# Optimization experiments

Hardware: AMD Instinct MI355X
Metric: run time of the kernel (lower is better)

Reference implementation:

```python
import jax, jax.numpy as jnp
import numpy as np

D = 64        # GatedGraphConv out_channels
N_LAYERS = 5  # number of stacked convs


def setup_inputs() -> dict:
    key = jax.random.key(0)
    ks = jax.random.split(key, 16)
    N, E, G = 100000, 1600000, 64
    s = 0.1
    inp = {
        'conv_weight': jax.random.normal(ks[0], (N_LAYERS, D, D), jnp.float32) * s,
        'gru_w_ih':    jax.random.normal(ks[1], (N_LAYERS, 3 * D, D), jnp.float32) * s,
        'gru_w_hh':    jax.random.normal(ks[2], (N_LAYERS, 3 * D, D), jnp.float32) * s,
        'gru_b_ih':    jax.random.normal(ks[3], (N_LAYERS, 3 * D), jnp.float32) * s,
        'gru_b_hh':    jax.random.normal(ks[4], (N_LAYERS, 3 * D), jnp.float32) * s,
        'fc1_w': jax.random.normal(ks[5], (32, D), jnp.float32) * s,
        'fc1_b': jax.random.normal(ks[6], (32,), jnp.float32) * s,
        'fc2_w': jax.random.normal(ks[7], (16, 32), jnp.float32) * s,
        'fc2_b': jax.random.normal(ks[8], (16,), jnp.float32) * s,
        'fc3_w': jax.random.normal(ks[9], (1, 16), jnp.float32) * s,
        'fc3_b': jax.random.normal(ks[10], (1,), jnp.float32) * s,
        'edge_index': jax.random.randint(ks[11], (2, E), 0, N, jnp.int64 if jax.config.jax_enable_x64 else jnp.int32),
        'batch': jnp.sort(jax.random.randint(ks[12], (N,), 0, G, jnp.int32)),
        'num_nodes': N,
        'num_graphs': G,
    }
    return inp


def _gru_cell(m, h, w_ih, w_hh, b_ih, b_hh):
    # torch.nn.GRUCell math; m: [N,D] input, h: [N,D] hidden
    gi = m @ w_ih.T + b_ih   # [N, 3D]
    gh = h @ w_hh.T + b_hh   # [N, 3D]
    i_r, i_z, i_n = jnp.split(gi, 3, axis=1)
    h_r, h_z, h_n = jnp.split(gh, 3, axis=1)
    r = jax.nn.sigmoid(i_r + h_r)
    z = jax.nn.sigmoid(i_z + h_z)
    n = jnp.tanh(i_n + r * h_n)
    return (1.0 - z) * n + z * h


def reference(conv_weight, gru_w_ih, gru_w_hh, gru_b_ih, gru_b_hh,
              fc1_w, fc1_b, fc2_w, fc2_b, fc3_w, fc3_b,
              edge_index, batch, num_nodes, num_graphs):
    src, dst = edge_index[0], edge_index[1]  # source_to_target flow
    # initial node features: zeros [N,8] zero-padded to D by GatedGraphConv
    x0 = jnp.zeros((num_nodes, D), jnp.float32)

    def step(x, params):
        w, wih, whh, bih, bhh = params
        m = x @ w                                        # [N, D]
        agg = jax.ops.segment_sum(m[src], dst, num_segments=num_nodes)  # scatter-add
        return _gru_cell(agg, x, wih, whh, bih, bhh), None

    x, _ = jax.lax.scan(step, x0,
                        (conv_weight, gru_w_ih, gru_w_hh, gru_b_ih, gru_b_hh))

    # scatter_add pooling over batch -> [num_graphs, D]
    g = jax.ops.segment_sum(x, batch, num_segments=num_graphs)
    h = jax.nn.elu(g @ fc1_w.T + fc1_b)
    h = jax.nn.elu(h @ fc2_w.T + fc2_b)
    return h @ fc3_w.T + fc3_b  # [num_graphs, 1]
```

## Files before the change

kernel.cpp:

```cpp
#include <hip/hip_runtime.h>
#include <math.h>

typedef _Float16 f16x2 __attribute__((ext_vector_type(2)));
typedef _Float16 f16x4 __attribute__((ext_vector_type(4)));
typedef _Float16 f16x8 __attribute__((ext_vector_type(8)));
typedef float f32x4 __attribute__((ext_vector_type(4)));

#define CBITS 10
#define FCHUNK 4096
#define MATSZ 13056
#define SEGSZ 2176
#define TABN 512
__device__ __forceinline__ int woff(int row) { return 64 * row + 8 * (row >> 1); }

__device__ __forceinline__ float sigmoidf_(float v) {
  return 1.0f / (1.0f + __expf(-v));
}
__device__ __forceinline__ float tanhf_(float v) {
  v = fminf(fmaxf(v, -15.f), 15.f);
  float e = __expf(2.f * v);
  return (e - 1.f) / (e + 1.f);
}
__device__ __forceinline__ float eluf_(float v) { return v > 0.f ? v : (__expf(v) - 1.f); }

__global__ __launch_bounds__(256) void histwprep_kernel(const int* __restrict__ dst,
                                                        int* __restrict__ bh, int E, int nfb,
                                                        const float* __restrict__ conv_w,
                                                        const float* __restrict__ w_ih,
                                                        const float* __restrict__ whh,
                                                        const float* __restrict__ b_ih,
                                                        const float* __restrict__ b_hh,
                                                        _Float16* __restrict__ wcS,
                                                        _Float16* __restrict__ whhS,
                                                        _Float16* __restrict__ tab,
                                                        float* __restrict__ gbuf, int gn) {
  __shared__ float sWt[64 * 68];
  __shared__ float sI[48 * 64];
  __shared__ float sh1[64], st[64], su[192], scons[256];
  __shared__ int h[128];
  const int t = threadIdx.x;
  if (blockIdx.x < nfb) {
    if (t < 128) h[t] = 0;
    __syncthreads();
    const int e0 = blockIdx.x * FCHUNK;
    int cnt = E - e0;
    if (cnt > FCHUNK) cnt = FCHUNK;
    for (int i = t; i < cnt; i += 256) atomicAdd(&h[dst[e0 + i] >> CBITS], 1);
    __syncthreads();
    if (t < 128) bh[blockIdx.x * 128 + t] = h[t];
    return;
  }
  const int bid = blockIdx.x - nfb;
  if (bid < 12) {
    const int l = 2 + (bid >> 2);
    const int j0 = (bid & 3) * 48;
    const float* W = conv_w + (size_t)l * 4096;
    const float* wi = w_ih + (size_t)l * 12288;
    _Float16* out = wcS + (size_t)l * MATSZ;
    for (int i = t; i < 4096; i += 256) sWt[(i & 63) * 68 + (i >> 6)] = W[i];
    for (int i = t; i < 3072; i += 256) sI[i] = wi[j0 * 64 + i];
    __syncthreads();
#pragma unroll
    for (int r = 0; r < 3; ++r) {
      int u = t + 256 * r;
      int j = u >> 4, cg = (u & 15) * 4;
      float4 a = {0.f, 0.f, 0.f, 0.f};
      for (int k = 0; k < 64; ++k) {
        float4 w = *(const float4*)(sWt + k * 68 + cg);
        float s = sI[j * 64 + k];
        a.x += w.x * s; a.y += w.y * s; a.z += w.z * s; a.w += w.w * s;
      }
      int row = j0 + j;
      f16x4 hv;
      hv[0] = (_Float16)a.x; hv[1] = (_Float16)a.y;
      hv[2] = (_Float16)a.z; hv[3] = (_Float16)a.w;
      *(f16x4*)(out + woff(row) + cg) = hv;
    }
  } else if (bid < 48) {
    int idx = (bid - 12) * 256 + t;
    if (idx >= 9216) return;
    int l = 2 + idx / 3072, rem = idx % 3072;
    int r = rem >> 4, c4 = (rem & 15) * 4;
    float4 v = *(const float4*)(whh + (size_t)l * 12288 + r * 64 + c4);
    f16x4 hv;
    hv[0] = (_Float16)v.x; hv[1] = (_Float16)v.y;
    hv[2] = (_Float16)v.z; hv[3] = (_Float16)v.w;
    *(f16x4*)(whhS + (size_t)l * MATSZ + woff(r) + c4) = hv;
  } else {
    for (int i = t; i < gn; i += 256) gbuf[i] = 0.f;
    if (t < 64) {
      float r = sigmoidf_(b_ih[t] + b_hh[t]);
      float z = sigmoidf_(b_ih[64 + t] + b_hh[64 + t]);
      float n = tanhf_(b_ih[128 + t] + r * b_hh[128 + t]);
      sh1[t] = (1.f - z) * n;
    }
    __syncthreads();
    if (t < 64) {
      const float* W1 = conv_w + 4096;
      float a = 0.f;
      for (int c = 0; c < 64; ++c) a += sh1[c] * W1[c * 64 + t];
      st[t] = a;
    }
    __syncthreads();
    if (t < 192) {
      const float* wih1 = w_ih + 12288;
      const float* whh1 = whh + 12288;
      float uacc = 0.f, sg = 0.f;
      for (int k = 0; k < 64; ++k) {
        uacc += wih1[t * 64 + k] * st[k];
        sg += whh1[t * 64 + k] * sh1[k];
      }
      su[t] = uacc;
      const float* bi1 = b_ih + 192;
      const float* bh1 = b_hh + 192;
      if (t < 128) {
        scons[t] = sg + bi1[t] + bh1[t];
      } else {
        scons[t] = bi1[t];
        scons[t + 64] = sg + bh1[t];
      }
    }
    __syncthreads();
    for (int idx = t; idx < TABN * 64; idx += 256) {
      int dgi = idx >> 6, j = idx & 63;
      float dg = (float)dgi;
      float r = sigmoidf_(dg * su[j] + scons[j]);
      float z = sigmoidf_(dg * su[64 + j] + scons[64 + j]);
      float n = tanhf_(dg * su[128 + j] + scons[128 + j] + r * scons[192 + j]);
      tab[idx] = (_Float16)(n + z * (sh1[j] - n));
    }
  }
}

__global__ __launch_bounds__(64) void chunkscan_kernel(const int* __restrict__ bh,
                                                       int* __restrict__ cbase,
                                                       int* __restrict__ tot, int nfb) {
  const int b = blockIdx.x;
  const int lane = threadIdx.x;
  int carry = 0;
  for (int base = 0; base < nfb; base += 64) {
    int kk = base + lane;
    int v = (kk < nfb) ? bh[kk * 128 + b] : 0;
    int s = v;
#pragma unroll
    for (int o = 1; o < 64; o <<= 1) {
      int u = __shfl_up(s, o);
      if (lane >= o) s += u;
    }
    if (kk < nfb) cbase[kk * 128 + b] = carry + s - v;
    carry += __shfl(s, 63);
  }
  if (lane == 0) tot[b] = carry;
}

__global__ __launch_bounds__(256) void bucket_fill_kernel(const int* __restrict__ src,
                                                          const int* __restrict__ dst,
                                                          const int* __restrict__ bh,
                                                          const int* __restrict__ cbase,
                                                          const int* __restrict__ tot,
                                                          unsigned* __restrict__ pairs,
                                                          int E) {
  __shared__ uint2 staged[FCHUNK];
  __shared__ int h[128], lbase[128], gbase[128], lcur[128], cs[128];
  const int t = threadIdx.x;
  const int k = blockIdx.x;
  int vtot = 0;
  if (t < 128) {
    vtot = tot[t];
    cs[t] = vtot;
  }
  __syncthreads();
  for (int o = 1; o < 128; o <<= 1) {
    int a = (t < 128 && t >= o) ? cs[t - o] : 0;
    __syncthreads();
    if (t < 128) cs[t] += a;
    __syncthreads();
  }
  if (t < 128) {
    int bucketbase = cs[t] - vtot;
    gbase[t] = bucketbase + cbase[k * 128 + t];
    int myh = bh[k * 128 + t];
    h[t] = myh;
    lcur[t] = myh;
  }
  __syncthreads();
  for (int o = 1; o < 128; o <<= 1) {
    int a = (t < 128 && t >= o) ? lcur[t - o] : 0;
    __syncthreads();
    if (t < 128) lcur[t] += a;
    __syncthreads();
  }
  if (t < 128) {
    int ex = lcur[t] - h[t];
    lbase[t] = ex;
    lcur[t] = ex;
  }
  __syncthreads();
  const int e0 = k * FCHUNK;
  int cnt = E - e0;
  if (cnt > FCHUNK) cnt = FCHUNK;
  for (int i = t; i < cnt; i += 256) {
    int d = dst[e0 + i];
    int b = d >> CBITS;
    int p = atomicAdd(&lcur[b], 1);
    staged[p] = make_uint2((unsigned)src[e0 + i], (unsigned)d);
  }
  __syncthreads();
  for (int i = t; i < cnt; i += 256) {
    uint2 pr = staged[i];
    int b = (int)(pr.y >> CBITS);
    pairs[gbase[b] + (i - lbase[b])] = (pr.x << CBITS) | (pr.y & ((1u << CBITS) - 1));
  }
}

__global__ __launch_bounds__(256) void csr_build_kernel(const unsigned* __restrict__ pairs,
                                                        const int* __restrict__ tot,
                                                        int* __restrict__ offs,
                                                        int* __restrict__ srcs,
                                                        unsigned short* __restrict__ deg16,
                                                        int N, int E) {
  const int b = blockIdx.x, t = threadIdx.x;
  const int nbase = b << CBITS;
  __shared__ int deg[1024];
  __shared__ int ssc[256];
  __shared__ int cs[128];
  if (t < 128) cs[t] = tot[t];
  __syncthreads();
  for (int o = 1; o < 128; o <<= 1) {
    int a = (t < 128 && t >= o) ? cs[t - o] : 0;
    __syncthreads();
    if (t < 128) cs[t] += a;
    __syncthreads();
  }
  const int beg = (b > 0) ? cs[b - 1] : 0;
  const int end = cs[b];
  __syncthreads();
  for (int i = t; i < 1024; i += 256) deg[i] = 0;
  __syncthreads();
  for (int e = beg + t; e < end; e += 256) atomicAdd(&deg[pairs[e] & 1023], 1);
  __syncthreads();
  int d0 = deg[4 * t], d1 = deg[4 * t + 1], d2 = deg[4 * t + 2], d3 = deg[4 * t + 3];
  int s = d0 + d1 + d2 + d3;
  ssc[t] = s;
  __syncthreads();
  for (int o = 1; o < 256; o <<= 1) {
    int a = (t >= o) ? ssc[t - o] : 0;
    __syncthreads();
    ssc[t] += a;
    __syncthreads();
  }
  int base = beg + ssc[t] - s;
  int c0 = base, c1 = c0 + d0, c2 = c1 + d1, c3 = c2 + d2;
  if (nbase + 4 * t + 0 < N) { offs[nbase + 4 * t + 0] = c0; deg16[nbase + 4 * t + 0] = (unsigned short)d0; }
  if (nbase + 4 * t + 1 < N) { offs[nbase + 4 * t + 1] = c1; deg16[nbase + 4 * t + 1] = (unsigned short)d1; }
  if (nbase + 4 * t + 2 < N) { offs[nbase + 4 * t + 2] = c2; deg16[nbase + 4 * t + 2] = (unsigned short)d2; }
  if (nbase + 4 * t + 3 < N) { offs[nbase + 4 * t + 3] = c3; deg16[nbase + 4 * t + 3] = (unsigned short)d3; }
  deg[4 * t] = c0; deg[4 * t + 1] = c1; deg[4 * t + 2] = c2; deg[4 * t + 3] = c3;
  if (b == 0 && t == 0) offs[N] = E;
  if (b == 0 && t < 64) srcs[E + t] = 0;
  __syncthreads();
  for (int e = beg + t; e < end; e += 256) {
    unsigned p = pairs[e];
    int pos = atomicAdd(&deg[p & 1023], 1);
    srcs[pos] = (int)(p >> CBITS);
  }
}

__global__ __launch_bounds__(256) void agg2_kernel(const _Float16* __restrict__ tab,
                                                   const unsigned short* __restrict__ deg16,
                                                   const int* __restrict__ offs,
                                                   const int* __restrict__ srcs,
                                                   _Float16* __restrict__ aggh, int N) {
  int wave = threadIdx.x >> 6, lane = threadIdx.x & 63;
  int v = blockIdx.x * 4 + wave;
  if (v >= N) return;
  const int beg = offs[v], end = offs[v + 1];
  const int deg = end - beg;
  const int og = lane >> 3;
  const int lp = lane & 7;
  f16x8 acc = {};
  for (int base = 0; base < deg; base += 64) {
    const int cnt = min(64, deg - base);
    const int cnt8 = (cnt + 7) & ~7;
    int sidx = 0;
    if (lane < cnt8) sidx = srcs[beg + base + lane];
    int s0 = __shfl(sidx, og);
    int d0 = min((int)deg16[s0], TABN - 1);
    f16x8 cur = *(const f16x8*)(tab + d0 * 64 + lp * 8);
    int e = 0;
    for (; e + 8 < cnt; e += 8) {
      int sn = __shfl(sidx, e + 8 + og);
      int dn = min((int)deg16[sn], TABN - 1);
      f16x8 nxt = *(const f16x8*)(tab + dn * 64 + lp * 8);
      acc += cur;
      cur = nxt;
    }
    if (e + og < cnt) acc += cur;
  }
#pragma unroll
  for (int off = 8; off < 64; off <<= 1) {
    union { f16x8 h; int i[4]; } a, b;
    a.h = acc;
#pragma unroll
    for (int w = 0; w < 4; ++w) b.i[w] = __shfl_xor(a.i[w], off);
    acc += b.h;
  }
  if (og == 0) *(f16x8*)(aggh + (size_t)v * 64 + lp * 8) = acc;
}

__global__ __launch_bounds__(256) void agg_kernel(const _Float16* __restrict__ xh,
                                                  const int* __restrict__ offs,
                                                  const int* __restrict__ srcs,
                                                  _Float16* __restrict__ aggh, int N) {
  int wave = threadIdx.x >> 6, lane = threadIdx.x & 63;
  int v = blockIdx.x * 4 + wave;
  if (v >= N) return;
  const int beg = offs[v], end = offs[v + 1];
  const int deg = end - beg;
  const int og = lane >> 3;
  const int lp = lane & 7;
  f16x8 acc = {};
  for (int base = 0; base < deg; base += 64) {
    const int cnt = min(64, deg - base);
    const int cnt8 = (cnt + 7) & ~7;
    int sidx = 0;
    if (lane < cnt8) sidx = srcs[beg + base + lane];
    int s0 = __shfl(sidx, og);
    f16x8 cur = *(const f16x8*)(xh + (size_t)s0 * 64 + lp * 8);
    int e = 0;
    for (; e + 8 < cnt; e += 8) {
      int sn = __shfl(sidx, e + 8 + og);
      f16x8 nxt = *(const f16x8*)(xh + (size_t)sn * 64 + lp * 8);
      acc += cur;
      cur = nxt;
    }
    if (e + og < cnt) acc += cur;
  }
#pragma unroll
  for (int off = 8; off < 64; off <<= 1) {
    union { f16x8 h; int i[4]; } a, b;
    a.h = acc;
#pragma unroll
    for (int w = 0; w < 4; ++w) b.i[w] = __shfl_xor(a.i[w], off);
    acc += b.h;
  }
  if (og == 0) *(f16x8*)(aggh + (size_t)v * 64 + lp * 8) = acc;
}

template <bool TABH>
__device__ __forceinline__ void gru_body(const _Float16* __restrict__ aggh,
                                         const _Float16* __restrict__ xh_in,
                                         const unsigned short* __restrict__ deg16,
                                         const _Float16* __restrict__ tab,
                                         _Float16* __restrict__ xh_out,
                                         const _Float16* __restrict__ wcS,
                                         const _Float16* __restrict__ whhS,
                                         const float* __restrict__ b_ih,
                                         const float* __restrict__ b_hh,
                                         int N, int tiles) {
  __shared__ _Float16 sW[2 * 3 * SEGSZ];
  const int t = threadIdx.x;
  const int half = blockIdx.x & 1;
  for (int i = t; i < 1632; i += 256) {
    int mat = (i >= 816) ? 1 : 0;
    int rem = i - mat * 816;
    int seg = rem / 272;
    int u = rem % 272;
    const _Float16* srcp = (mat ? whhS : wcS) + woff(half * 32 + seg * 64) + u * 8;
    *(f16x8*)(sW + (mat * 3 + seg) * SEGSZ + u * 8) = *(const f16x8*)srcp;
  }
  __syncthreads();
  const int wave = t >> 6, lane = t & 63;
  const int q = lane >> 4, c = lane & 15;
  float bRZ[2], bZZ[2], bIN[2], bHN[2];
#pragma unroll
  for (int p = 0; p < 2; ++p) {
    int d = (half * 2 + p) * 16 + c;
    bRZ[p] = b_ih[d] + b_hh[d];
    bZZ[p] = b_ih[64 + d] + b_hh[64 + d];
    bIN[p] = b_ih[128 + d];
    bHN[p] = b_hh[128 + d];
  }
  f16x8 idf[2];
#pragma unroll
  for (int p = 0; p < 2; ++p) {
    int tgt = p * 16 + c - q * 8;
#pragma unroll
    for (int j = 0; j < 8; ++j) idf[p][j] = (j == tgt) ? (_Float16)1.0f : (_Float16)0.0f;
  }
#pragma unroll 1
  for (int tile = blockIdx.x >> 1; tile < tiles; tile += gridDim.x >> 1) {
    const int nb0 = tile * 64 + wave * 16;
    const size_t rowbase = (size_t)(nb0 + c) * 64;
    f16x8 aA[2], aH[2];
    if (TABH) {
      int dg = min((int)deg16[nb0 + c], TABN - 1);
#pragma unroll
      for (int ks = 0; ks < 2; ++ks) {
        aA[ks] = *(const f16x8*)(aggh + rowbase + ks * 32 + q * 8);
        aH[ks] = *(const f16x8*)(tab + dg * 64 + ks * 32 + q * 8);
      }
    } else {
#pragma unroll
      for (int ks = 0; ks < 2; ++ks) {
        aA[ks] = *(const f16x8*)(aggh + rowbase + ks * 32 + q * 8);
        aH[ks] = *(const f16x8*)(xh_in + rowbase + ks * 32 + q * 8);
      }
    }
    f32x4 aR[2], aZ[2], aN[2], aHNa[2], aHO[2];
#pragma unroll
    for (int p = 0; p < 2; ++p) {
      aR[p] = (f32x4){bRZ[p], bRZ[p], bRZ[p], bRZ[p]};
      aZ[p] = (f32x4){bZZ[p], bZZ[p], bZZ[p], bZZ[p]};
      aN[p] = (f32x4){bIN[p], bIN[p], bIN[p], bIN[p]};
      aHNa[p] = (f32x4){bHN[p], bHN[p], bHN[p], bHN[p]};
      aHO[p] = (f32x4){0.f, 0.f, 0.f, 0.f};
    }
#pragma unroll
    for (int ks = 0; ks < 2; ++ks) {
      const int colo = ks * 32 + q * 8;
#pragma unroll
      for (int p = 0; p < 2; ++p) {
        const int lr = p * 16 + c;
        const int ro = 64 * lr + 8 * (lr >> 1);
        f16x8 bWr = *(const f16x8*)(sW + 0 * SEGSZ + ro + colo);
        f16x8 bWz = *(const f16x8*)(sW + 1 * SEGSZ + ro + colo);
        f16x8 bWn = *(const f16x8*)(sW + 2 * SEGSZ + ro + colo);
        f16x8 bHr = *(const f16x8*)(sW + 3 * SEGSZ + ro + colo);
        f16x8 bHz = *(const f16x8*)(sW + 4 * SEGSZ + ro + colo);
        f16x8 bHn = *(const f16x8*)(sW + 5 * SEGSZ + ro + colo);
        aR[p] = __builtin_amdgcn_mfma_f32_16x16x32_f16(aA[ks], bWr, aR[p], 0, 0, 0);
        aR[p] = __builtin_amdgcn_mfma_f32_16x16x32_f16(aH[ks], bHr, aR[p], 0, 0, 0);
        aZ[p] = __builtin_amdgcn_mfma_f32_16x16x32_f16(aA[ks], bWz, aZ[p], 0, 0, 0);
        aZ[p] = __builtin_amdgcn_mfma_f32_16x16x32_f16(aH[ks], bHz, aZ[p], 0, 0, 0);
        aN[p] = __builtin_amdgcn_mfma_f32_16x16x32_f16(aA[ks], bWn, aN[p], 0, 0, 0);
        aHNa[p] = __builtin_amdgcn_mfma_f32_16x16x32_f16(aH[ks], bHn, aHNa[p], 0, 0, 0);
      }
    }
#pragma unroll
    for (int p = 0; p < 2; ++p)
      aHO[p] = __builtin_amdgcn_mfma_f32_16x16x32_f16(aH[half], idf[p], aHO[p], 0, 0, 0);
#pragma unroll
    for (int p = 0; p < 2; ++p) {
      int d = (half * 2 + p) * 16 + c;
#pragma unroll
      for (int r = 0; r < 4; ++r) {
        int node = nb0 + q * 4 + r;
        if (node < N) {
          float rr = sigmoidf_(aR[p][r]);
          float zz = sigmoidf_(aZ[p][r]);
          float nn = tanhf_(aN[p][r] + rr * aHNa[p][r]);
          float out = nn + zz * (aHO[p][r] - nn);
          xh_out[(size_t)node * 64 + d] = (_Float16)out;
        }
      }
    }
  }
}

__global__ __launch_bounds__(256) void gru_kernel(const _Float16* __restrict__ aggh,
                                                  const _Float16* __restrict__ xh_in,
                                                  _Float16* __restrict__ xh_out,
                                                  const _Float16* __restrict__ wcS,
                                                  const _Float16* __restrict__ whhS,
                                                  const float* __restrict__ b_ih,
                                                  const float* __restrict__ b_hh,
                                                  int N, int tiles) {
  gru_body<false>(aggh, xh_in, nullptr, nullptr, xh_out, wcS, whhS, b_ih, b_hh, N, tiles);
}

__global__ __launch_bounds__(256) void gru2_kernel(const _Float16* __restrict__ aggh,
                                                   const unsigned short* __restrict__ deg16,
                                                   const _Float16* __restrict__ tab,
                                                   _Float16* __restrict__ xh_out,
                                                   const _Float16* __restrict__ wcS,
                                                   const _Float16* __restrict__ whhS,
                                                   const float* __restrict__ b_ih,
                                                   const float* __restrict__ b_hh,
                                                   int N, int tiles) {
  gru_body<true>(aggh, nullptr, deg16, tab, xh_out, wcS, whhS, b_ih, b_hh, N, tiles);
}

__global__ __launch_bounds__(256) void pool_kernel(const _Float16* __restrict__ xh,
                                                   const int* __restrict__ batch,
                                                   float* __restrict__ g, int N) {
  int wave = threadIdx.x >> 6, lane = threadIdx.x & 63;
  int n0 = blockIdx.x * 64 + wave * 16;
  if (n0 >= N) return;
  int end = n0 + 16;
  if (end > N) end = N;
  int cur = batch[n0];
  float acc = 0.f;
  for (int n = n0; n < end; ++n) {
    int b = batch[n];
    if (b != cur) {
      atomicAdd(&g[(size_t)cur * 64 + lane], acc);
      acc = 0.f;
      cur = b;
    }
    acc += (float)xh[(size_t)n * 64 + lane];
  }
  atomicAdd(&g[(size_t)cur * 64 + lane], acc);
}

__global__ __launch_bounds__(256) void mlp_kernel(const float* __restrict__ g,
                                                  const float* __restrict__ w1,
                                                  const float* __restrict__ b1,
                                                  const float* __restrict__ w2,
                                                  const float* __restrict__ b2,
                                                  const float* __restrict__ w3,
                                                  const float* __restrict__ b3,
                                                  float* __restrict__ out, int G) {
  __shared__ float sG[64 * 64];
  __shared__ float sH1[64 * 32];
  __shared__ float sH2[64 * 16];
  int t = threadIdx.x;
  for (int i = t; i < G * 64; i += 256) sG[i] = g[i];
  __syncthreads();
  for (int o = t; o < G * 32; o += 256) {
    int gi = o >> 5, i = o & 31;
    float a = b1[i];
    for (int k = 0; k < 64; ++k) a += sG[gi * 64 + k] * w1[i * 64 + k];
    sH1[gi * 32 + i] = eluf_(a);
  }
  __syncthreads();
  for (int o = t; o < G * 16; o += 256) {
    int gi = o >> 4, i = o & 15;
    float a = b2[i];
    for (int k = 0; k < 32; ++k) a += sH1[gi * 32 + k] * w2[i * 32 + k];
    sH2[gi * 16 + i] = eluf_(a);
  }
  __syncthreads();
  for (int o = t; o < G; o += 256) {
    float a = b3[0];
    for (int k = 0; k < 16; ++k) a += sH2[o * 16 + k] * w3[k];
    out[o] = a;
  }
}

extern "C" void kernel_launch(void* const* d_in, const int* in_sizes, int n_in,
                              void* d_out, int out_size, void* d_ws, size_t ws_size,
                              hipStream_t stream) {
  const float* conv_w = (const float*)d_in[0];
  const float* w_ih = (const float*)d_in[1];
  const float* w_hh = (const float*)d_in[2];
  const float* b_ih = (const float*)d_in[3];
  const float* b_hh = (const float*)d_in[4];
  const float* fc1_w = (const float*)d_in[5];
  const float* fc1_b = (const float*)d_in[6];
  const float* fc2_w = (const float*)d_in[7];
  const float* fc2_b = (const float*)d_in[8];
  const float* fc3_w = (const float*)d_in[9];
  const float* fc3_b = (const float*)d_in[10];
  const int* ei = (const int*)d_in[11];
  const int* batch = (const int*)d_in[12];
  const int N = in_sizes[12];
  const int E = in_sizes[11] / 2;
  const int G = out_size;
  const int* src = ei;
  const int* dst = ei + E;
  const int nfb = (E + FCHUNK - 1) / FCHUNK;
  const int nbk = (N + 1023) >> CBITS;
  const int tiles = (N + 63) / 64;
  const int Npad = tiles * 64;

  char* ws = (char*)d_ws;
  size_t off = 0;
  auto alloc = [&](size_t bytes) -> void* {
    void* p = ws + off;
    off += (bytes + 255) & ~(size_t)255;
    return p;
  };
  _Float16* xhA = (_Float16*)alloc((size_t)Npad * 64 * 2);
  _Float16* xhB = (_Float16*)alloc((size_t)Npad * 64 * 2);
  _Float16* aggh = (_Float16*)alloc((size_t)Npad * 64 * 2);
  _Float16* wcS = (_Float16*)alloc((size_t)5 * MATSZ * 2);
  _Float16* whhS = (_Float16*)alloc((size_t)5 * MATSZ * 2);
  _Float16* h2tab = (_Float16*)alloc((size_t)TABN * 64 * 2);
  float* gbuf = (float*)alloc((size_t)G * 64 * 4);
  int* offs = (int*)alloc((size_t)(N + 1) * 4);
  int* srcs = (int*)alloc((size_t)(E + 64) * 4);
  unsigned short* deg16 = (unsigned short*)alloc((size_t)Npad * 2);
  unsigned* pairs = (unsigned*)alloc((size_t)E * 4);
  int* bh = (int*)alloc((size_t)nfb * 128 * 4);
  int* cbase = (int*)alloc((size_t)nfb * 128 * 4);
  int* tot = (int*)alloc(128 * 4);

  histwprep_kernel<<<nfb + 49, 256, 0, stream>>>(dst, bh, E, nfb, conv_w, w_ih, w_hh,
                                                 b_ih, b_hh, wcS, whhS, h2tab, gbuf, G * 64);
  chunkscan_kernel<<<128, 64, 0, stream>>>(bh, cbase, tot, nfb);
  bucket_fill_kernel<<<nfb, 256, 0, stream>>>(src, dst, bh, cbase, tot, pairs, E);
  csr_build_kernel<<<nbk, 256, 0, stream>>>(pairs, tot, offs, srcs, deg16, N, E);

  agg2_kernel<<<(N + 3) / 4, 256, 0, stream>>>(h2tab, deg16, offs, srcs, aggh, N);
  gru2_kernel<<<768, 256, 0, stream>>>(aggh, deg16, h2tab, xhA, wcS + 2 * MATSZ,
                                       whhS + 2 * MATSZ, b_ih + 2 * 192, b_hh + 2 * 192,
                                       N, tiles);
  _Float16* cur = xhA;
  _Float16* nxt = xhB;
  for (int l = 3; l < 5; ++l) {
    agg_kernel<<<(N + 3) / 4, 256, 0, stream>>>(cur, offs, srcs, aggh, N);
    gru_kernel<<<768, 256, 0, stream>>>(aggh, cur, nxt, wcS + (size_t)l * MATSZ,
                                        whhS + (size_t)l * MATSZ, b_ih + (size_t)l * 192,
                                        b_hh + (size_t)l * 192, N, tiles);
    _Float16* tmp = cur; cur = nxt; nxt = tmp;
  }

  pool_kernel<<<(N + 63) / 64, 256, 0, stream>>>(cur, batch, gbuf, N);
  mlp_kernel<<<1, 256, 0, stream>>>(gbuf, fc1_w, fc1_b, fc2_w, fc2_b, fc3_w, fc3_b,
                                    (float*)d_out, G);
}
```

Measured before the change: 381.6 us.

## Fuse graph pooling into final GRU layer and batch gather loads in aggregation

The last GRU layer now accumulates its outputs directly into the per-graph pooling buffer with segmented atomic adds, instead of writing node features and running a separate pool kernel. This removes one kernel launch and a full write and re-read of the final node feature array. Separately, the aggregation kernels issue all up to eight row gathers per 64-edge chunk before accumulating, replacing the one-ahead prefetch loop to expose more memory-level parallelism. The cost is more registers per thread in the gather kernels and more atomics issued from the GRU epilogue, since each lane handles only four nodes.

```diff
diff --git a/kernel.cpp b/kernel.cpp
--- a/kernel.cpp
+++ b/kernel.cpp
@@ -282,20 +282,22 @@
   for (int base = 0; base < deg; base += 64) {
     const int cnt = min(64, deg - base);
     const int cnt8 = (cnt + 7) & ~7;
+    const int steps = cnt8 >> 3;
     int sidx = 0;
     if (lane < cnt8) sidx = srcs[beg + base + lane];
-    int s0 = __shfl(sidx, og);
-    int d0 = min((int)deg16[s0], TABN - 1);
-    f16x8 cur = *(const f16x8*)(tab + d0 * 64 + lp * 8);
-    int e = 0;
-    for (; e + 8 < cnt; e += 8) {
-      int sn = __shfl(sidx, e + 8 + og);
-      int dn = min((int)deg16[sn], TABN - 1);
-      f16x8 nxt = *(const f16x8*)(tab + dn * 64 + lp * 8);
-      acc += cur;
-      cur = nxt;
-    }
-    if (e + og < cnt) acc += cur;
+    f16x8 rows[8];
+#pragma unroll
+    for (int s = 0; s < 8; ++s) {
+      if (s < steps) {
+        int sn = __shfl(sidx, s * 8 + og);
+        int dn = min((int)deg16[sn], TABN - 1);
+        rows[s] = *(const f16x8*)(tab + dn * 64 + lp * 8);
+      }
+    }
+#pragma unroll
+    for (int s = 0; s < 8; ++s) {
+      if (s * 8 + og < cnt) acc += rows[s];
+    }
   }
 #pragma unroll
   for (int off = 8; off < 64; off <<= 1) {
@@ -323,18 +325,21 @@
   for (int base = 0; base < deg; base += 64) {
     const int cnt = min(64, deg - base);
     const int cnt8 = (cnt + 7) & ~7;
+    const int steps = cnt8 >> 3;
     int sidx = 0;
     if (lane < cnt8) sidx = srcs[beg + base + lane];
-    int s0 = __shfl(sidx, og);
-    f16x8 cur = *(const f16x8*)(xh + (size_t)s0 * 64 + lp * 8);
-    int e = 0;
-    for (; e + 8 < cnt; e += 8) {
-      int sn = __shfl(sidx, e + 8 + og);
-      f16x8 nxt = *(const f16x8*)(xh + (size_t)sn * 64 + lp * 8);
-      acc += cur;
-      cur = nxt;
-    }
-    if (e + og < cnt) acc += cur;
+    f16x8 rows[8];
+#pragma unroll
+    for (int s = 0; s < 8; ++s) {
+      if (s < steps) {
+        int sn = __shfl(sidx, s * 8 + og);
+        rows[s] = *(const f16x8*)(xh + (size_t)sn * 64 + lp * 8);
+      }
+    }
+#pragma unroll
+    for (int s = 0; s < 8; ++s) {
+      if (s * 8 + og < cnt) acc += rows[s];
+    }
   }
 #pragma unroll
   for (int off = 8; off < 64; off <<= 1) {
@@ -347,12 +352,14 @@
   if (og == 0) *(f16x8*)(aggh + (size_t)v * 64 + lp * 8) = acc;
 }
 
-template <bool TABH>
+template <bool TABH, bool POOL>
 __device__ __forceinline__ void gru_body(const _Float16* __restrict__ aggh,
                                          const _Float16* __restrict__ xh_in,
                                          const unsigned short* __restrict__ deg16,
                                          const _Float16* __restrict__ tab,
                                          _Float16* __restrict__ xh_out,
+                                         const int* __restrict__ batch,
+                                         float* __restrict__ gbuf,
                                          const _Float16* __restrict__ wcS,
                                          const _Float16* __restrict__ whhS,
                                          const float* __restrict__ b_ih,
@@ -440,9 +447,19 @@
 #pragma unroll
     for (int p = 0; p < 2; ++p)
       aHO[p] = __builtin_amdgcn_mfma_f32_16x16x32_f16(aH[half], idf[p], aHO[p], 0, 0, 0);
+    int bb[4];
+    if (POOL) {
+#pragma unroll
+      for (int r = 0; r < 4; ++r) {
+        int node = nb0 + q * 4 + r;
+        bb[r] = (node < N) ? batch[node] : -1;
+      }
+    }
 #pragma unroll
     for (int p = 0; p < 2; ++p) {
       int d = (half * 2 + p) * 16 + c;
+      float pacc = 0.f;
+      int pg = -1;
 #pragma unroll
       for (int r = 0; r < 4; ++r) {
         int node = nb0 + q * 4 + r;
@@ -451,9 +468,19 @@
           float zz = sigmoidf_(aZ[p][r]);
           float nn = tanhf_(aN[p][r] + rr * aHNa[p][r]);
           float out = nn + zz * (aHO[p][r] - nn);
-          xh_out[(size_t)node * 64 + d] = (_Float16)out;
+          if (!POOL) {
+            xh_out[(size_t)node * 64 + d] = (_Float16)out;
+          } else {
+            if (bb[r] != pg) {
+              if (pg >= 0) atomicAdd(&gbuf[(size_t)pg * 64 + d], pacc);
+              pacc = 0.f;
+              pg = bb[r];
+            }
+            pacc += out;
+          }
         }
       }
+      if (POOL && pg >= 0) atomicAdd(&gbuf[(size_t)pg * 64 + d], pacc);
     }
   }
 }
@@ -466,7 +493,8 @@
                                                   const float* __restrict__ b_ih,
                                                   const float* __restrict__ b_hh,
                                                   int N, int tiles) {
-  gru_body<false>(aggh, xh_in, nullptr, nullptr, xh_out, wcS, whhS, b_ih, b_hh, N, tiles);
+  gru_body<false, false>(aggh, xh_in, nullptr, nullptr, xh_out, nullptr, nullptr,
+                         wcS, whhS, b_ih, b_hh, N, tiles);
 }
 
 __global__ __launch_bounds__(256) void gru2_kernel(const _Float16* __restrict__ aggh,
@@ -478,29 +506,21 @@
                                                    const float* __restrict__ b_ih,
                                                    const float* __restrict__ b_hh,
                                                    int N, int tiles) {
-  gru_body<true>(aggh, nullptr, deg16, tab, xh_out, wcS, whhS, b_ih, b_hh, N, tiles);
-}
-
-__global__ __launch_bounds__(256) void pool_kernel(const _Float16* __restrict__ xh,
+  gru_body<true, false>(aggh, nullptr, deg16, tab, xh_out, nullptr, nullptr,
+                        wcS, whhS, b_ih, b_hh, N, tiles);
+}
+
+__global__ __launch_bounds__(256) void gru4_kernel(const _Float16* __restrict__ aggh,
+                                                   const _Float16* __restrict__ xh_in,
                                                    const int* __restrict__ batch,
-                                                   float* __restrict__ g, int N) {
-  int wave = threadIdx.x >> 6, lane = threadIdx.x & 63;
-  int n0 = blockIdx.x * 64 + wave * 16;
-  if (n0 >= N) return;
-  int end = n0 + 16;
-  if (end > N) end = N;
-  int cur = batch[n0];
-  float acc = 0.f;
-  for (int n = n0; n < end; ++n) {
-    int b = batch[n];
-    if (b != cur) {
-      atomicAdd(&g[(size_t)cur * 64 + lane], acc);
-      acc = 0.f;
-      cur = b;
-    }
-    acc += (float)xh[(size_t)n * 64 + lane];
-  }
-  atomicAdd(&g[(size_t)cur * 64 + lane], acc);
+                                                   float* __restrict__ gbuf,
+                                                   const _Float16* __restrict__ wcS,
+                                                   const _Float16* __restrict__ whhS,
+                                                   const float* __restrict__ b_ih,
+                                                   const float* __restrict__ b_hh,
+                                                   int N, int tiles) {
+  gru_body<false, true>(aggh, xh_in, nullptr, nullptr, nullptr, batch, gbuf,
+                        wcS, whhS, b_ih, b_hh, N, tiles);
 }
 
 __global__ __launch_bounds__(256) void mlp_kernel(const float* __restrict__ g,
@@ -596,17 +616,14 @@
   gru2_kernel<<<768, 256, 0, stream>>>(aggh, deg16, h2tab, xhA, wcS + 2 * MATSZ,
                                        whhS + 2 * MATSZ, b_ih + 2 * 192, b_hh + 2 * 192,
                                        N, tiles);
-  _Float16* cur = xhA;
-  _Float16* nxt = xhB;
-  for (int l = 3; l < 5; ++l) {
-    agg_kernel<<<(N + 3) / 4, 256, 0, stream>>>(cur, offs, srcs, aggh, N);
-    gru_kernel<<<768, 256, 0, stream>>>(aggh, cur, nxt, wcS + (size_t)l * MATSZ,
-                                        whhS + (size_t)l * MATSZ, b_ih + (size_t)l * 192,
-                                        b_hh + (size_t)l * 192, N, tiles);
-    _Float16* tmp = cur; cur = nxt; nxt = tmp;
-  }
-
-  pool_kernel<<<(N + 63) / 64, 256, 0, stream>>>(cur, batch, gbuf, N);
+  agg_kernel<<<(N + 3) / 4, 256, 0, stream>>>(xhA, offs, srcs, aggh, N);
+  gru_kernel<<<768, 256, 0, stream>>>(aggh, xhA, xhB, wcS + 3 * MATSZ, whhS + 3 * MATSZ,
+                                      b_ih + 3 * 192, b_hh + 3 * 192, N, tiles);
+  agg_kernel<<<(N + 3) / 4, 256, 0, stream>>>(xhB, offs, srcs, aggh, N);
+  gru4_kernel<<<768, 256, 0, stream>>>(aggh, xhB, batch, gbuf, wcS + 4 * MATSZ,
+                                       whhS + 4 * MATSZ, b_ih + 4 * 192, b_hh + 4 * 192,
+                                       N, tiles);
+
   mlp_kernel<<<1, 256, 0, stream>>>(gbuf, fc1_w, fc1_b, fc2_w, fc2_b, fc3_w, fc3_b,
                                     (float*)d_out, G);
 }
```

New measurement: 486.7 us. 27.6% more time.
